# Kernel tuning notes

Measured on AMD Instinct MI355X. Metric: run time of the kernel, lower is better.

The kernel has to match this reference:

```python
import jax, jax.numpy as jnp
import numpy as np

def setup_inputs() -> dict:
    key = jax.random.key(0)
    QKV = jax.random.normal(key, (3, 2, 8, 4096, 64), dtype=jnp.float32)
    return {"QKV": QKV}

def reference(QKV):
    Q, K, V = QKV[0], QKV[1], QKV[2]            # each [B, H, N, d]
    scores = jnp.einsum('bhnd,bhmd->bhnm', Q, K)  # full N x N score matrix (no scaling, matching source)
    attn = jax.nn.softmax(scores, axis=-1)
    return jnp.einsum('bhnm,bhmd->bhnd', attn, V)
```

## Files before the change

### kernel.cpp

```cpp
#include <hip/hip_runtime.h>


typedef _Float16 f16x8 __attribute__((ext_vector_type(8)));
typedef _Float16 f16x2 __attribute__((ext_vector_type(2)));
typedef short s16x8 __attribute__((ext_vector_type(8)));
typedef short s16x4 __attribute__((ext_vector_type(4)));
typedef float f32x4 __attribute__((ext_vector_type(4)));
typedef unsigned u32x4 __attribute__((ext_vector_type(4)));

#define NHEADS 16
#define SEQ 4096
#define HDIM 64
#define BR 128
#define NH 2
#define BC 64
#define KP 72
#define NSPLIT 2
#define MPAD 4.0f

__device__ __forceinline__ float fast_exp2(float x) {
#if __has_builtin(__builtin_amdgcn_exp2f)
  return __builtin_amdgcn_exp2f(x);
#else
  return exp2f(x);
#endif
}

__device__ __forceinline__ f16x2 pkrtz(float a, float b) {
  return __builtin_bit_cast(f16x2, __builtin_amdgcn_cvt_pkrtz(a, b));
}

__device__ __forceinline__ unsigned short f2bf(float f) {
  unsigned u = __builtin_bit_cast(unsigned, f);
  u += 0x7fffu + ((u >> 16) & 1u);
  return (unsigned short)(u >> 16);
}

__device__ __forceinline__ unsigned bfpack2(float a, float b) {
#if __has_builtin(__builtin_amdgcn_perm)
  return __builtin_amdgcn_perm(__builtin_bit_cast(unsigned, b),
                               __builtin_bit_cast(unsigned, a), 0x07060302u);
#else
  return (__builtin_bit_cast(unsigned, b) & 0xffff0000u) |
         (__builtin_bit_cast(unsigned, a) >> 16);
#endif
}

__device__ __forceinline__ void gload16(const void* g, void* l) {
  __builtin_amdgcn_global_load_lds(
      (const __attribute__((address_space(1))) unsigned int*)g,
      (__attribute__((address_space(3))) unsigned int*)l, 16, 0, 0);
}

__global__ __launch_bounds__(256) void prep(const float* __restrict__ QKV,
                                            _Float16* __restrict__ K16,
                                            short* __restrict__ Vt) {
  const size_t tensElems = (size_t)NHEADS * SEQ * HDIM;
  __shared__ __align__(16) short T[64 * KP];
  if (blockIdx.x < 2048) {
    const float* Kf = QKV + tensElems;
    size_t i = ((size_t)blockIdx.x * 256 + threadIdx.x) * 8;
    float4 a = *(const float4*)(Kf + i);
    float4 b = *(const float4*)(Kf + i + 4);
    union { f16x8 v; f16x2 h2[4]; } u;
    u.h2[0] = pkrtz(a.x, a.y);
    u.h2[1] = pkrtz(a.z, a.w);
    u.h2[2] = pkrtz(b.x, b.y);
    u.h2[3] = pkrtz(b.z, b.w);
    size_t r = (i >> 6) & 63, c = (i >> 3) & 7;
    size_t dst = (i >> 12) * 4096 + r * 64 + (((c + r) & 7) << 3);
    *(f16x8*)(K16 + dst) = u.v;
  } else {
    const int vb = blockIdx.x - 2048;
    const int bh = vb >> 6;
    const int nt = vb & 63;
    const float* Vh = QKV + 2 * tensElems + (size_t)bh * SEQ * HDIM +
                      (size_t)nt * 64 * HDIM;
    const int t = threadIdx.x;
    #pragma unroll
    for (int p = 0; p < 4; ++p) {
      int idx = t + p * 256;
      int row = idx >> 4, c4 = (idx & 15) << 2;
      float4 v = *(const float4*)(Vh + row * HDIM + c4);
      s16x4 h;
      h[0] = (short)f2bf(v.x); h[1] = (short)f2bf(v.y);
      h[2] = (short)f2bf(v.z); h[3] = (short)f2bf(v.w);
      *(s16x4*)&T[row * KP + c4] = h;
    }
    __syncthreads();
    short* outT = Vt + ((size_t)bh * 64 + nt) * 4096;
    const int p0 = 2 * t;
    const int d0 = p0 >> 3;
    const int k0 = (((p0 & 7) - d0) & 7) << 3;
    const int k1 = ((((p0 + 1) & 7) - d0) & 7) << 3;
    s16x8 o0, o1;
    #pragma unroll
    for (int j = 0; j < 8; ++j) o0[j] = T[(k0 + j) * KP + d0];
    #pragma unroll
    for (int j = 0; j < 8; ++j) o1[j] = T[(k1 + j) * KP + d0];
    *(s16x8*)(outT + p0 * 8) = o0;
    *(s16x8*)(outT + p0 * 8 + 8) = o1;
  }
}

template <int NS>
__global__ __launch_bounds__(256) void combineN(const _Float16* __restrict__ Op,
                                                const float2* __restrict__ Ml,
                                                float* __restrict__ O) {
  const size_t tensElems = (size_t)NHEADS * SEQ * HDIM;
  size_t t = (size_t)blockIdx.x * 256 + threadIdx.x;
  size_t row = t >> 3;
  int seg = (int)(t & 7) << 3;
  float2 s[NS];
  #pragma unroll
  for (int i = 0; i < NS; ++i) s[i] = Ml[(size_t)i * NHEADS * SEQ + row];
  float Ms = s[0].x;
  #pragma unroll
  for (int i = 1; i < NS; ++i) Ms = fmaxf(Ms, s[i].x);
  float a[NS], tot = 0.f;
  #pragma unroll
  for (int i = 0; i < NS; ++i) {
    a[i] = fast_exp2(s[i].x - Ms) * s[i].y;
    tot += a[i];
  }
  float inv = 1.0f / tot;
  float r[8] = {0.f, 0.f, 0.f, 0.f, 0.f, 0.f, 0.f, 0.f};
  #pragma unroll
  for (int i = 0; i < NS; ++i) {
    f16x8 o = *(const f16x8*)(Op + (size_t)i * tensElems + row * HDIM + seg);
    float w = a[i] * inv;
    #pragma unroll
    for (int j = 0; j < 8; ++j) r[j] += (float)o[j] * w;
  }
  float4 r0{r[0], r[1], r[2], r[3]}, r1{r[4], r[5], r[6], r[7]};
  *(float4*)(O + row * HDIM + seg) = r0;
  *(float4*)(O + row * HDIM + seg + 4) = r1;
}

template <bool PRE, bool SPLIT>
__global__ __launch_bounds__(256, 2) void flash_attn(const float* __restrict__ QKV,
                                                     const _Float16* __restrict__ K16g,
                                                     const short* __restrict__ Vt16,
                                                     float* __restrict__ Out,
                                                     _Float16* __restrict__ Opart,
                                                     float2* __restrict__ Ml) {
  const size_t headElems = (size_t)SEQ * HDIM;
  const size_t tensElems = (size_t)NHEADS * headElems;
  const int bh = blockIdx.x & 15;
  const int qt = blockIdx.x >> 4;
  const int split = SPLIT ? blockIdx.y : 0;
  const int nsp = SPLIT ? (int)gridDim.y : 1;
  const int ktN = (SEQ / BC) / nsp;
  const int ktBeg = split * ktN;

  const float* Q = QKV + (size_t)bh * headElems;
  const float* Kf = QKV + tensElems + (size_t)bh * headElems;
  const float* Vf = QKV + 2 * tensElems + (size_t)bh * headElems;
  const _Float16* Kg16 = K16g + (size_t)bh * headElems;
  const short* Vg16 = Vt16 + (size_t)bh * headElems;
  float* O = Out + (size_t)bh * headElems;

  const int tid = threadIdx.x;
  const int wave = tid >> 6;
  const int lane = tid & 63;
  const int g = lane >> 4;
  const int l16 = lane & 15;

  __shared__ __align__(16) _Float16 KsB[2][64 * 64];
  __shared__ __align__(16) short VsB[2][64 * 64];

  const float LOG2E = 1.4426950408889634f;
  const int qbase = qt * BR + wave * (16 * NH);
  f16x8 qf[NH][2];
  #pragma unroll
  for (int h = 0; h < NH; ++h) {
    const float* qp = Q + (size_t)(qbase + h * 16 + l16) * HDIM + g * 8;
    #pragma unroll
    for (int c = 0; c < 2; ++c) {
      float4 a = *(const float4*)(qp + c * 32);
      float4 b = *(const float4*)(qp + c * 32 + 4);
      union { f16x8 v; f16x2 h2[4]; } u;
      u.h2[0] = pkrtz(a.x * LOG2E, a.y * LOG2E);
      u.h2[1] = pkrtz(a.z * LOG2E, a.w * LOG2E);
      u.h2[2] = pkrtz(b.x * LOG2E, b.y * LOG2E);
      u.h2[3] = pkrtz(b.z * LOG2E, b.w * LOG2E);
      qf[h][c] = u.v;
    }
  }

  const int rbase = 8 * (l16 >> 2) + 4 * (l16 & 1) + ((l16 >> 1) & 1);
  const int so = tid << 4;

  auto stage = [&](int buf, int kt) {
    if constexpr (PRE) {
      const char* kg = (const char*)Kg16 + (size_t)kt * 8192 + so;
      const char* vg = (const char*)Vg16 + (size_t)kt * 8192 + so;
      char* kl = (char*)&KsB[buf][0] + (wave << 10);
      char* vl = (char*)&VsB[buf][0] + (wave << 10);
      gload16(kg, kl);
      gload16(kg + 4096, kl + 4096);
      gload16(vg, vl);
      gload16(vg + 4096, vl + 4096);
    } else {
      _Float16* Kd = KsB[buf];
      short* Vd = VsB[buf];
      const int sr = tid >> 2;
      const int s = tid & 3;
      const float* kg = Kf + (size_t)(kt * BC + sr) * HDIM + s * 16;
      float4 a = *(const float4*)(kg), b = *(const float4*)(kg + 4);
      float4 c = *(const float4*)(kg + 8), d = *(const float4*)(kg + 12);
      union { f16x8 v; f16x2 h2[4]; } ka, kb;
      ka.h2[0] = pkrtz(a.x, a.y);
      ka.h2[1] = pkrtz(a.z, a.w);
      ka.h2[2] = pkrtz(b.x, b.y);
      ka.h2[3] = pkrtz(b.z, b.w);
      kb.h2[0] = pkrtz(c.x, c.y);
      kb.h2[1] = pkrtz(c.z, c.w);
      kb.h2[2] = pkrtz(d.x, d.y);
      kb.h2[3] = pkrtz(d.z, d.w);
      *(f16x8*)&Kd[sr * 64 + (((2 * s + sr) & 7) << 3)] = ka.v;
      *(f16x8*)&Kd[sr * 64 + (((2 * s + 1 + sr) & 7) << 3)] = kb.v;
      const float* vg = Vf + (size_t)(kt * BC + sr) * HDIM + s * 16;
      float4 va = *(const float4*)(vg), vb = *(const float4*)(vg + 4);
      float4 vc = *(const float4*)(vg + 8), vd = *(const float4*)(vg + 12);
      float vv[16] = {va.x, va.y, va.z, va.w, vb.x, vb.y, vb.z, vb.w,
                      vc.x, vc.y, vc.z, vc.w, vd.x, vd.y, vd.z, vd.w};
      #pragma unroll
      for (int j = 0; j < 16; ++j) {
        int dd = s * 16 + j;
        Vd[dd * 64 + ((((sr >> 3) + dd) & 7) << 3) + (sr & 7)] =
            (short)f2bf(vv[j]);
      }
    }
  };

  f32x4 acc[NH][4];
  #pragma unroll
  for (int h = 0; h < NH; ++h)
    #pragma unroll
    for (int nt = 0; nt < 4; ++nt)
      #pragma unroll
      for (int i = 0; i < 4; ++i) acc[h][nt][i] = 0.f;
  float l_[NH] = {0.f, 0.f};
  float negM[NH] = {0.f, 0.f};

  stage(0, ktBeg);
  int cur = 0;

  for (int it = 0; it < ktN; ++it) {
    __syncthreads();
    if (it + 1 < ktN) stage(cur ^ 1, ktBeg + it + 1);
    const _Float16* Kb = KsB[cur];
    const short* Vb = VsB[cur];

    if (it == 0) {
      float mx[NH];
      #pragma unroll
      for (int h = 0; h < NH; ++h) mx[h] = -3.0e38f;
      #pragma unroll
      for (int jt = 0; jt < 4; ++jt) {
        const int r = rbase + ((jt >> 1) << 5) + ((jt & 1) << 1);
        const int ka = r * 64 + (((g + r) & 7) << 3);
        f16x8 k0 = *(const f16x8*)&Kb[ka];
        f16x8 k1 = *(const f16x8*)&Kb[ka ^ 32];
        #pragma unroll
        for (int h = 0; h < NH; ++h) {
          f32x4 z;
          z[0] = z[1] = z[2] = z[3] = 0.f;
          z = __builtin_amdgcn_mfma_f32_16x16x32_f16(k0, qf[h][0], z, 0, 0, 0);
          z = __builtin_amdgcn_mfma_f32_16x16x32_f16(k1, qf[h][1], z, 0, 0, 0);
          mx[h] = fmaxf(mx[h], fmaxf(fmaxf(z[0], z[1]), fmaxf(z[2], z[3])));
        }
      }
      #pragma unroll
      for (int h = 0; h < NH; ++h) {
        float m2 = fmaxf(mx[h], __shfl_xor(mx[h], 16));
        m2 = fmaxf(m2, __shfl_xor(m2, 32));
        negM[h] = -(m2 + MPAD);
      }
    }

    #pragma unroll
    for (int half = 0; half < 2; ++half) {
      u32x4 Wp[NH];
      #pragma unroll
      for (int jt2 = 0; jt2 < 2; ++jt2) {
        const int r = rbase + (half << 5) + (jt2 << 1);
        const int ka = r * 64 + (((g + r) & 7) << 3);
        f16x8 k0 = *(const f16x8*)&Kb[ka];
        f16x8 k1 = *(const f16x8*)&Kb[ka ^ 32];
        #pragma unroll
        for (int h = 0; h < NH; ++h) {
          f32x4 z;
          z[0] = z[1] = z[2] = z[3] = negM[h];
          z = __builtin_amdgcn_mfma_f32_16x16x32_f16(k0, qf[h][0], z, 0, 0, 0);
          z = __builtin_amdgcn_mfma_f32_16x16x32_f16(k1, qf[h][1], z, 0, 0, 0);
          float p0 = fast_exp2(z[0]);
          float p1 = fast_exp2(z[1]);
          float p2 = fast_exp2(z[2]);
          float p3 = fast_exp2(z[3]);
          l_[h] += (p0 + p1) + (p2 + p3);
          Wp[h][jt2] = bfpack2(p0, p2);
          Wp[h][jt2 + 2] = bfpack2(p1, p3);
        }
      }
      __builtin_amdgcn_s_setprio(1);
      #pragma unroll
      for (int nt = 0; nt < 4; ++nt) {
        const int row = nt * 16 + l16;
        int va = row * 64 + (((g + row) & 7) << 3);
        if (half) va ^= 32;
        s16x8 v = *(const s16x8*)&Vb[va];
        #pragma unroll
        for (int h = 0; h < NH; ++h) {
          acc[h][nt] = __builtin_amdgcn_mfma_f32_16x16x32_bf16(
              __builtin_bit_cast(s16x8, Wp[h]), v, acc[h][nt], 0, 0, 0);
        }
      }
      __builtin_amdgcn_s_setprio(0);
    }

    cur ^= 1;
  }

  #pragma unroll
  for (int h = 0; h < NH; ++h) {
    float lf = l_[h];
    lf += __shfl_xor(lf, 16);
    lf += __shfl_xor(lf, 32);
    float linv = 1.0f / lf;
    if constexpr (SPLIT) {
      if (g == 0) {
        Ml[(size_t)split * NHEADS * SEQ + (size_t)bh * SEQ + qbase + h * 16 + l16] =
            float2{-negM[h], lf};
      }
      _Float16* op = Opart + (size_t)split * tensElems + (size_t)bh * headElems;
      #pragma unroll
      for (int ri = 0; ri < 4; ++ri) {
        float lB = __shfl(linv, 4 * g + ri);
        const int row = qbase + h * 16 + 4 * g + ri;
        #pragma unroll
        for (int nt = 0; nt < 4; ++nt)
          op[(size_t)row * HDIM + nt * 16 + l16] = (_Float16)(acc[h][nt][ri] * lB);
      }
    } else {
      #pragma unroll
      for (int ri = 0; ri < 4; ++ri) {
        float lB = __shfl(linv, 4 * g + ri);
        const int row = qbase + h * 16 + 4 * g + ri;
        #pragma unroll
        for (int nt = 0; nt < 4; ++nt)
          O[(size_t)row * HDIM + nt * 16 + l16] = acc[h][nt][ri] * lB;
      }
    }
  }
}

extern "C" void kernel_launch(void* const* d_in, const int* in_sizes, int n_in,
                              void* d_out, int out_size, void* d_ws, size_t ws_size,
                              hipStream_t stream) {
  const float* QKV = (const float*)d_in[0];
  float* Out = (float*)d_out;
  const size_t tensElems = (size_t)NHEADS * SEQ * HDIM;
  const size_t k16Bytes = tensElems * sizeof(_Float16);
  const size_t vtBytes = tensElems * sizeof(short);
  const size_t opBytes = (size_t)NSPLIT * tensElems * sizeof(_Float16);
  const size_t mlBytes = (size_t)NSPLIT * NHEADS * SEQ * 8;

  dim3 block(256);

  if (ws_size >= k16Bytes + vtBytes + opBytes + mlBytes) {
    _Float16* K16 = (_Float16*)d_ws;
    short* Vt16 = (short*)((char*)d_ws + k16Bytes);
    _Float16* Opart = (_Float16*)((char*)d_ws + k16Bytes + vtBytes);
    float2* Ml = (float2*)((char*)d_ws + k16Bytes + vtBytes + opBytes);
    hipLaunchKernelGGL(prep, dim3(3072), block, 0, stream, QKV, K16, Vt16);
    hipLaunchKernelGGL((flash_attn<true, true>), dim3(NHEADS * (SEQ / BR), NSPLIT),
                       block, 0, stream, QKV, K16, Vt16, Out, Opart, Ml);
    hipLaunchKernelGGL((combineN<NSPLIT>), dim3((NHEADS * SEQ * HDIM / 8) / 256),
                       block, 0, stream, Opart, Ml, Out);
  } else {
    hipLaunchKernelGGL((flash_attn<false, false>), dim3(NHEADS * (SEQ / BR)), block,
                       0, stream, QKV, (const _Float16*)nullptr,
                       (const short*)nullptr, Out, (_Float16*)nullptr,
                       (float2*)nullptr);
  }
}
```

Measured before the change: 168.2 us.

## Compute softmax row sums via MFMA with ones vector and stagger halves per wave

Replaces the per-lane VALU accumulation of the softmax denominator with an extra bf16 MFMA that multiplies the packed probabilities by a ones vector, so the row sums land already in the accumulator layout and no cross-lane shuffles are needed at the end. It also alternates the order of the two key halves between odd and even waves, likely to spread LDS bank access and MFMA/VALU contention. The cost is two extra MFMAs per half-iteration and row sums taken from bf16-rounded probabilities, which is consistent with the numerator but changes precision slightly.

```diff
diff --git a/kernel.cpp b/kernel.cpp
--- a/kernel.cpp
+++ b/kernel.cpp
@@ -187,6 +187,10 @@
       qf[h][c] = u.v;
     }
   }
+
+  s16x8 onesb;
+  #pragma unroll
+  for (int j = 0; j < 8; ++j) onesb[j] = (short)0x3F80;
 
   const int rbase = 8 * (l16 >> 2) + 4 * (l16 & 1) + ((l16 >> 1) & 1);
   const int so = tid << 4;
@@ -235,13 +239,16 @@
   };
 
   f32x4 acc[NH][4];
-  #pragma unroll
-  for (int h = 0; h < NH; ++h)
+  f32x4 acc_l[NH];
+  #pragma unroll
+  for (int h = 0; h < NH; ++h) {
     #pragma unroll
     for (int nt = 0; nt < 4; ++nt)
       #pragma unroll
       for (int i = 0; i < 4; ++i) acc[h][nt][i] = 0.f;
-  float l_[NH] = {0.f, 0.f};
+    #pragma unroll
+    for (int i = 0; i < 4; ++i) acc_l[h][i] = 0.f;
+  }
   float negM[NH] = {0.f, 0.f};
 
   stage(0, ktBeg);
@@ -281,7 +288,8 @@
     }
 
     #pragma unroll
-    for (int half = 0; half < 2; ++half) {
+    for (int hh = 0; hh < 2; ++hh) {
+      const int half = hh ^ (wave & 1);
       u32x4 Wp[NH];
       #pragma unroll
       for (int jt2 = 0; jt2 < 2; ++jt2) {
@@ -299,12 +307,16 @@
           float p1 = fast_exp2(z[1]);
           float p2 = fast_exp2(z[2]);
           float p3 = fast_exp2(z[3]);
-          l_[h] += (p0 + p1) + (p2 + p3);
           Wp[h][jt2] = bfpack2(p0, p2);
           Wp[h][jt2 + 2] = bfpack2(p1, p3);
         }
       }
       __builtin_amdgcn_s_setprio(1);
+      #pragma unroll
+      for (int h = 0; h < NH; ++h) {
+        acc_l[h] = __builtin_amdgcn_mfma_f32_16x16x32_bf16(
+            __builtin_bit_cast(s16x8, Wp[h]), onesb, acc_l[h], 0, 0, 0);
+      }
       #pragma unroll
       for (int nt = 0; nt < 4; ++nt) {
         const int row = nt * 16 + l16;
@@ -325,19 +337,21 @@
 
   #pragma unroll
   for (int h = 0; h < NH; ++h) {
-    float lf = l_[h];
-    lf += __shfl_xor(lf, 16);
-    lf += __shfl_xor(lf, 32);
-    float linv = 1.0f / lf;
     if constexpr (SPLIT) {
-      if (g == 0) {
-        Ml[(size_t)split * NHEADS * SEQ + (size_t)bh * SEQ + qbase + h * 16 + l16] =
-            float2{-negM[h], lf};
+      float nm[4];
+      #pragma unroll
+      for (int ri = 0; ri < 4; ++ri) nm[ri] = __shfl(negM[h], 4 * g + ri);
+      if (l16 == 0) {
+        #pragma unroll
+        for (int ri = 0; ri < 4; ++ri) {
+          Ml[(size_t)split * NHEADS * SEQ + (size_t)bh * SEQ + qbase + h * 16 +
+             4 * g + ri] = float2{-nm[ri], acc_l[h][ri]};
+        }
       }
       _Float16* op = Opart + (size_t)split * tensElems + (size_t)bh * headElems;
       #pragma unroll
       for (int ri = 0; ri < 4; ++ri) {
-        float lB = __shfl(linv, 4 * g + ri);
+        float lB = 1.0f / acc_l[h][ri];
         const int row = qbase + h * 16 + 4 * g + ri;
         #pragma unroll
         for (int nt = 0; nt < 4; ++nt)
@@ -346,7 +360,7 @@
     } else {
       #pragma unroll
       for (int ri = 0; ri < 4; ++ri) {
-        float lB = __shfl(linv, 4 * g + ri);
+        float lB = 1.0f / acc_l[h][ri];
         const int row = qbase + h * 16 + 4 * g + ri;
         #pragma unroll
         for (int nt = 0; nt < 4; ++nt)
```

Result: faster. 163.6 us (-2.8%).
